# Kernel tuning notes

Hardware: AMD Instinct MI355X
Metric: run time of the kernel (lower is better)

## Reference

```python
import jax, jax.numpy as jnp
import numpy as np

NEG = jnp.float32(-1e30)  # finite stand-in for -inf in masked max
SLOPE = 0.01              # F.leaky_relu default negative slope


def _lrelu(v):
    return jnp.where(v >= 0, v, SLOPE * v)


def _mlp(pts, w1, b1, w2, b2, w3, b3):
    # pts: [2, N] -> [64, N]; 1x1 Conv1d == pointwise linear over channel dim
    z = _lrelu(w1 @ pts + b1[:, None])
    z = _lrelu(w2 @ z + b2[:, None])
    z = _lrelu(w3 @ z + b3[:, None])
    return z


def setup_inputs() -> dict:
    key = jax.random.key(0)
    ks = jax.random.split(key, 10)
    B, C, H, W = 4, 19, 256, 256
    x = jax.random.randint(ks[0], (B, C, H, W), 0, 2, dtype=jnp.int32)
    # grid exactly as in the torch module: meshgrid of two linspaces, flattened
    g = np.array(np.meshgrid(np.linspace(-1, 1, 256), np.linspace(-1, 1, 256),
                             sparse=False)).astype(np.float32)  # [2,256,256]
    grid = jnp.asarray(g.reshape(2, -1))  # [2, 65536]
    w1 = jax.random.normal(ks[1], (64, 2), jnp.float32) * 0.5
    b1 = jax.random.normal(ks[2], (64,), jnp.float32) * 0.1
    w2 = jax.random.normal(ks[3], (64, 64), jnp.float32) * 0.125
    b2 = jax.random.normal(ks[4], (64,), jnp.float32) * 0.1
    w3 = jax.random.normal(ks[5], (64, 64), jnp.float32) * 0.125
    b3 = jax.random.normal(ks[6], (64,), jnp.float32) * 0.1
    fcw = jax.random.normal(ks[7], (512, 64 * C), jnp.float32)
    fcb = jax.random.normal(ks[8], (512,), jnp.float32) * 0.1
    return {"x": x, "grid": grid, "w1": w1, "b1": b1, "w2": w2, "b2": b2,
            "w3": w3, "b3": b3, "fcw": fcw, "fcb": fcb}


def reference(x, grid, w1, b1, w2, b2, w3, b3, fcw, fcb):
    B, C = x.shape[0], x.shape[1]
    # Pointwise MLP on the shared grid once (grid identical for all b,c)
    feats = _mlp(grid, w1, b1, w2, b2, w3, b3)                 # [64, N]
    # Fallback feature for empty masks: MLP on a single zero point
    zero_feat = _mlp(jnp.zeros((2, 1), feats.dtype),
                     w1, b1, w2, b2, w3, b3)[:, 0]             # [64]
    mask = (x.reshape(B, C, -1) == 1)                          # [B, C, N]
    # Masked max over the ragged point sets, fully vectorized
    masked = jnp.where(mask[:, :, None, :], feats[None, None], NEG)
    z = jnp.max(masked, axis=-1)                               # [B, C, 64]
    empty = ~jnp.any(mask, axis=-1)                            # [B, C]
    z = jnp.where(empty[..., None], zero_feat, z)
    flat = z.reshape(B, C * 64)                                # channel-major cat
    # EqualLinear: weight scaled by 1/sqrt(in_dim) (lr_mul=1)
    scale = jnp.float32(1.0 / np.sqrt(C * 64))
    out = flat @ (fcw * scale).T + fcb                         # [B, 512]
    return jnp.repeat(out[:, None, :], 18, axis=1)             # [B, 18, 512]
```

## Files before the change

### kernel.cpp

```cpp
#include <hip/hip_runtime.h>

#define NPTS  65536
#define NBC   76
#define NREP  8
#define KEYN  4864

__device__ __forceinline__ float lrelu(float v) { return fmaxf(v, 0.01f * v); }

__device__ __forceinline__ unsigned fkey(float f) {
  unsigned u = __float_as_uint(f);
  return (u & 0x80000000u) ? ~u : (u | 0x80000000u);
}
__device__ __forceinline__ float fdec(unsigned k) {
  return (k & 0x80000000u) ? __uint_as_float(k & 0x7fffffffu) : __uint_as_float(~k);
}

__global__ __launch_bounds__(512, 8) void k1_fused(
    const int* __restrict__ x, const float* __restrict__ grid,
    const float* __restrict__ w1, const float* __restrict__ b1,
    const float* __restrict__ w2, const float* __restrict__ b2,
    const float* __restrict__ w3, const float* __restrict__ b3,
    unsigned* __restrict__ keys)
{
  __shared__ unsigned zt1[64 * 68];
  __shared__ unsigned zt2[64 * 68];
  __shared__ unsigned long long mbits[NBC];

  const int t    = threadIdx.x;
  const int lane = t & 63;
  const int wv   = t >> 6;
  const int n0   = blockIdx.x * 64;

  #pragma unroll
  for (int i = 0; i < 10; ++i) {
    int bc = wv + 8 * i;
    if (bc < NBC) {
      int v = x[(bc << 16) + n0 + lane];
      unsigned long long m = __ballot(v == 1);
      if (lane == 0) mbits[bc] = m;
    }
  }

  const int jb = __builtin_amdgcn_readfirstlane(wv * 8);

  {
    float g0 = grid[n0 + lane];
    float g1 = grid[NPTS + n0 + lane];
    #pragma unroll
    for (int jj = 0; jj < 8; ++jj) {
      int j = jb + jj;
      float z = lrelu(w1[2 * j] * g0 + w1[2 * j + 1] * g1 + b1[j]);
      zt1[j * 68 + lane] = __float_as_uint(z);
    }
  }
  __syncthreads();

  float acc[8];

  #pragma unroll
  for (int jj = 0; jj < 8; ++jj) acc[jj] = b2[jb + jj];
  #pragma unroll 4
  for (int k = 0; k < 64; ++k) {
    float zv = __uint_as_float(zt1[k * 68 + lane]);
    #pragma unroll
    for (int jj = 0; jj < 8; ++jj) acc[jj] += w2[(jb + jj) * 64 + k] * zv;
  }
  #pragma unroll
  for (int jj = 0; jj < 8; ++jj)
    zt2[(jb + jj) * 68 + lane] = __float_as_uint(lrelu(acc[jj]));
  __syncthreads();

  #pragma unroll
  for (int jj = 0; jj < 8; ++jj) acc[jj] = b3[jb + jj];
  #pragma unroll 4
  for (int k = 0; k < 64; ++k) {
    float zv = __uint_as_float(zt2[k * 68 + lane]);
    #pragma unroll
    for (int jj = 0; jj < 8; ++jj) acc[jj] += w3[(jb + jj) * 64 + k] * zv;
  }
  #pragma unroll
  for (int jj = 0; jj < 8; ++jj)
    zt1[(jb + jj) * 68 + lane] = fkey(lrelu(acc[jj]));
  __syncthreads();

  const int kq = t & 31, bg = t >> 5;
  const int bcbase = bg * 5;

  unsigned mlo[5], mhi[5];
  #pragma unroll
  for (int ii = 0; ii < 5; ++ii) {
    int bc = bcbase + ii;
    unsigned long long m = (bc < NBC) ? mbits[bc] : 0ull;
    mlo[ii] = (unsigned)m;
    mhi[ii] = (unsigned)(m >> 32);
  }

  unsigned uacc[5][2];
  #pragma unroll
  for (int ii = 0; ii < 5; ++ii) { uacc[ii][0] = 0u; uacc[ii][1] = 0u; }

  #pragma unroll 2
  for (int np = 0; np < 8; ++np) {
    const int n = np * 4;
    uint4 lo0 = *reinterpret_cast<const uint4*>(&zt1[kq * 68 + n]);
    uint4 lo1 = *reinterpret_cast<const uint4*>(&zt1[(kq + 32) * 68 + n]);
    uint4 hi0 = *reinterpret_cast<const uint4*>(&zt1[kq * 68 + n + 32]);
    uint4 hi1 = *reinterpret_cast<const uint4*>(&zt1[(kq + 32) * 68 + n + 32]);
    #pragma unroll
    for (int ii = 0; ii < 5; ++ii) {
      unsigned sl0 = (unsigned)((int)(mlo[ii] << (31 - n)) >> 31);
      unsigned sl1 = (unsigned)((int)(mlo[ii] << (30 - n)) >> 31);
      unsigned sl2 = (unsigned)((int)(mlo[ii] << (29 - n)) >> 31);
      unsigned sl3 = (unsigned)((int)(mlo[ii] << (28 - n)) >> 31);
      unsigned sh0 = (unsigned)((int)(mhi[ii] << (31 - n)) >> 31);
      unsigned sh1 = (unsigned)((int)(mhi[ii] << (30 - n)) >> 31);
      unsigned sh2 = (unsigned)((int)(mhi[ii] << (29 - n)) >> 31);
      unsigned sh3 = (unsigned)((int)(mhi[ii] << (28 - n)) >> 31);
      unsigned a0 = uacc[ii][0], a1 = uacc[ii][1];
      a0 = max(max(a0, lo0.x & sl0), lo0.y & sl1);
      a0 = max(max(a0, lo0.z & sl2), lo0.w & sl3);
      a0 = max(max(a0, hi0.x & sh0), hi0.y & sh1);
      a0 = max(max(a0, hi0.z & sh2), hi0.w & sh3);
      a1 = max(max(a1, lo1.x & sl0), lo1.y & sl1);
      a1 = max(max(a1, lo1.z & sl2), lo1.w & sl3);
      a1 = max(max(a1, hi1.x & sh0), hi1.y & sh1);
      a1 = max(max(a1, hi1.z & sh2), hi1.w & sh3);
      uacc[ii][0] = a0; uacc[ii][1] = a1;
    }
  }

  unsigned* krep = keys + (blockIdx.x & (NREP - 1)) * KEYN;
  #pragma unroll
  for (int ii = 0; ii < 5; ++ii) {
    int bc = bcbase + ii;
    if (bc < NBC) {
      unsigned v0 = uacc[ii][0], v1 = uacc[ii][1];
      if (v0) atomicMax(&krep[bc * 64 + kq], v0);
      if (v1) atomicMax(&krep[bc * 64 + kq + 32], v1);
    }
  }
}

__global__ __launch_bounds__(256) void k2_fc(
    const unsigned* __restrict__ keys,
    const float* __restrict__ b1, const float* __restrict__ w2,
    const float* __restrict__ b2, const float* __restrict__ w3,
    const float* __restrict__ b3,
    const float* __restrict__ fcw, const float* __restrict__ fcb,
    float* __restrict__ out)
{
  __shared__ float flat[4864];
  __shared__ float za[64], zb[64], zf[64];
  const int t = threadIdx.x;

  if (t < 64) za[t] = lrelu(b1[t]);
  __syncthreads();
  if (t < 64) {
    float s = b2[t];
    #pragma unroll 8
    for (int k = 0; k < 64; ++k) s += w2[t * 64 + k] * za[k];
    zb[t] = lrelu(s);
  }
  __syncthreads();
  if (t < 64) {
    float s = b3[t];
    #pragma unroll 8
    for (int k = 0; k < 64; ++k) s += w3[t * 64 + k] * zb[k];
    zf[t] = lrelu(s);
  }
  __syncthreads();

  for (int idx = t; idx < 4864; idx += 256) {
    unsigned m = keys[idx];
    #pragma unroll
    for (int r = 1; r < NREP; ++r) m = max(m, keys[r * KEYN + idx]);
    flat[idx] = m ? fdec(m) : zf[idx & 63];
  }
  __syncthreads();

  const int wv = t >> 6, lane = t & 63;
  const int o = blockIdx.x * 4 + wv;
  const float* wrow = fcw + o * 1216;
  float fa0 = 0.f, fa1 = 0.f, fa2 = 0.f, fa3 = 0.f;
  #pragma unroll
  for (int i = 0; i < 19; ++i) {
    int jj = i * 64 + lane;
    float wvv = wrow[jj];
    fa0 += wvv * flat[jj];
    fa1 += wvv * flat[1216 + jj];
    fa2 += wvv * flat[2432 + jj];
    fa3 += wvv * flat[3648 + jj];
  }
  #pragma unroll
  for (int off = 32; off > 0; off >>= 1) {
    fa0 += __shfl_xor(fa0, off);
    fa1 += __shfl_xor(fa1, off);
    fa2 += __shfl_xor(fa2, off);
    fa3 += __shfl_xor(fa3, off);
  }
  const float scale = 0.028676966733820225f;
  float cb = fcb[o];
  if (lane < 18) {
    out[(0 * 18 + lane) * 512 + o] = fa0 * scale + cb;
    out[(1 * 18 + lane) * 512 + o] = fa1 * scale + cb;
    out[(2 * 18 + lane) * 512 + o] = fa2 * scale + cb;
    out[(3 * 18 + lane) * 512 + o] = fa3 * scale + cb;
  }
}

extern "C" void kernel_launch(void* const* d_in, const int* in_sizes, int n_in,
                              void* d_out, int out_size, void* d_ws, size_t ws_size,
                              hipStream_t stream)
{
  const int*   x    = (const int*)d_in[0];
  const float* grid = (const float*)d_in[1];
  const float* w1   = (const float*)d_in[2];
  const float* b1   = (const float*)d_in[3];
  const float* w2   = (const float*)d_in[4];
  const float* b2   = (const float*)d_in[5];
  const float* w3   = (const float*)d_in[6];
  const float* b3   = (const float*)d_in[7];
  const float* fcw  = (const float*)d_in[8];
  const float* fcb  = (const float*)d_in[9];
  float* out = (float*)d_out;

  unsigned* keys = (unsigned*)d_ws;

  hipMemsetAsync(d_ws, 0, NREP * KEYN * sizeof(unsigned), stream);
  hipLaunchKernelGGL(k1_fused, dim3(1024), dim3(512), 0, stream,
                     x, grid, w1, b1, w2, b2, w3, b3, keys);
  hipLaunchKernelGGL(k2_fc, dim3(128), dim3(256), 0, stream,
                     keys, b1, w2, b2, w3, b3, fcw, fcb, out);
}
```

Baseline: 142.2 us.

## Run pointwise MLP layers on fp16 MFMA and pack max keys as 16-bit pairs

```diff
diff --git a/kernel.cpp b/kernel.cpp
--- a/kernel.cpp
+++ b/kernel.cpp
@@ -5,14 +5,28 @@
 #define NREP  8
 #define KEYN  4864
 
+typedef _Float16 f16;
+typedef __fp16   h16x2 __attribute__((ext_vector_type(2)));
+typedef _Float16 f16x8 __attribute__((ext_vector_type(8)));
+typedef float    f32x4 __attribute__((ext_vector_type(4)));
+
 __device__ __forceinline__ float lrelu(float v) { return fmaxf(v, 0.01f * v); }
 
-__device__ __forceinline__ unsigned fkey(float f) {
-  unsigned u = __float_as_uint(f);
-  return (u & 0x80000000u) ? ~u : (u | 0x80000000u);
-}
-__device__ __forceinline__ float fdec(unsigned k) {
-  return (k & 0x80000000u) ? __uint_as_float(k & 0x7fffffffu) : __uint_as_float(~k);
+__device__ __forceinline__ unsigned pkrtz(float lo, float hi) {
+  h16x2 p = __builtin_amdgcn_cvt_pkrtz(lo, hi);
+  return __builtin_bit_cast(unsigned, p);
+}
+__device__ __forceinline__ unsigned pkey(unsigned u) {
+  unsigned t = (u >> 15) & 0x00010001u;
+  return u ^ (0x80008000u | (t * 0x7FFFu));
+}
+__device__ __forceinline__ unsigned pkmax(unsigned a, unsigned b) {
+  unsigned d;
+  asm("v_pk_max_u16 %0, %1, %2" : "=v"(d) : "v"(a), "v"(b));
+  return d;
+}
+__device__ __forceinline__ unsigned sext1(unsigned x, int b) {
+  return (unsigned)(((int)(x << (31 - b))) >> 31);
 }
 
 __global__ __launch_bounds__(512, 8) void k1_fused(
@@ -22,121 +36,144 @@
     const float* __restrict__ w3, const float* __restrict__ b3,
     unsigned* __restrict__ keys)
 {
-  __shared__ unsigned zt1[64 * 68];
-  __shared__ unsigned zt2[64 * 68];
+  __shared__ __align__(16) unsigned char smem[36864];
   __shared__ unsigned long long mbits[NBC];
+  f16* zA  = (f16*)(smem);
+  f16* zB  = (f16*)(smem + 9216);
+  f16* wf2 = (f16*)(smem + 18432);
+  f16* wf3 = (f16*)(smem + 27648);
+  unsigned* zkey = (unsigned*)(smem + 18432);
 
   const int t    = threadIdx.x;
   const int lane = t & 63;
   const int wv   = t >> 6;
   const int n0   = blockIdx.x * 64;
 
+  int xv[10];
   #pragma unroll
   for (int i = 0; i < 10; ++i) {
     int bc = wv + 8 * i;
-    if (bc < NBC) {
-      int v = x[(bc << 16) + n0 + lane];
-      unsigned long long m = __ballot(v == 1);
-      if (lane == 0) mbits[bc] = m;
-    }
-  }
-
-  const int jb = __builtin_amdgcn_readfirstlane(wv * 8);
-
-  {
-    float g0 = grid[n0 + lane];
-    float g1 = grid[NPTS + n0 + lane];
-    #pragma unroll
-    for (int jj = 0; jj < 8; ++jj) {
-      int j = jb + jj;
-      float z = lrelu(w1[2 * j] * g0 + w1[2 * j + 1] * g1 + b1[j]);
-      zt1[j * 68 + lane] = __float_as_uint(z);
-    }
-  }
-  __syncthreads();
-
-  float acc[8];
-
-  #pragma unroll
-  for (int jj = 0; jj < 8; ++jj) acc[jj] = b2[jb + jj];
-  #pragma unroll 4
-  for (int k = 0; k < 64; ++k) {
-    float zv = __uint_as_float(zt1[k * 68 + lane]);
-    #pragma unroll
-    for (int jj = 0; jj < 8; ++jj) acc[jj] += w2[(jb + jj) * 64 + k] * zv;
-  }
-  #pragma unroll
-  for (int jj = 0; jj < 8; ++jj)
-    zt2[(jb + jj) * 68 + lane] = __float_as_uint(lrelu(acc[jj]));
-  __syncthreads();
-
-  #pragma unroll
-  for (int jj = 0; jj < 8; ++jj) acc[jj] = b3[jb + jj];
-  #pragma unroll 4
-  for (int k = 0; k < 64; ++k) {
-    float zv = __uint_as_float(zt2[k * 68 + lane]);
-    #pragma unroll
-    for (int jj = 0; jj < 8; ++jj) acc[jj] += w3[(jb + jj) * 64 + k] * zv;
-  }
-  #pragma unroll
-  for (int jj = 0; jj < 8; ++jj)
-    zt1[(jb + jj) * 68 + lane] = fkey(lrelu(acc[jj]));
-  __syncthreads();
-
-  const int kq = t & 31, bg = t >> 5;
-  const int bcbase = bg * 5;
-
-  unsigned mlo[5], mhi[5];
+    xv[i] = (bc < NBC) ? x[(bc << 16) + n0 + lane] : 0;
+  }
+
+  {
+    int ch = t >> 3, k0 = (t & 7) * 8;
+    const float4* s2 = (const float4*)(w2 + ch * 64 + k0);
+    float4 a = s2[0], b = s2[1];
+    *(uint4*)&wf2[ch * 72 + k0] =
+        make_uint4(pkrtz(a.x, a.y), pkrtz(a.z, a.w), pkrtz(b.x, b.y), pkrtz(b.z, b.w));
+    const float4* s3 = (const float4*)(w3 + ch * 64 + k0);
+    float4 c = s3[0], d = s3[1];
+    *(uint4*)&wf3[ch * 72 + k0] =
+        make_uint4(pkrtz(c.x, c.y), pkrtz(c.z, c.w), pkrtz(d.x, d.y), pkrtz(d.z, d.w));
+  }
+
+  {
+    float g0 = grid[n0 + lane], g1 = grid[NPTS + n0 + lane];
+    unsigned uo[4];
+    #pragma unroll
+    for (int p = 0; p < 4; ++p) {
+      int j = wv * 8 + p * 2;
+      float z0 = lrelu(w1[2 * j] * g0 + w1[2 * j + 1] * g1 + b1[j]);
+      float z1 = lrelu(w1[2 * j + 2] * g0 + w1[2 * j + 3] * g1 + b1[j + 1]);
+      uo[p] = pkrtz(z0, z1);
+    }
+    *(uint4*)&zA[lane * 72 + wv * 8] = make_uint4(uo[0], uo[1], uo[2], uo[3]);
+  }
+  __syncthreads();
+
+  const int chb = (wv & 3) * 16, pth = (wv >> 2) * 32;
+  const int c15 = lane & 15, q = lane >> 4;
+  const int chq = chb + q * 4;
+  const int pt0 = pth + c15, pt1 = pth + 16 + c15;
+
+  f32x4 acc0, acc1;
+
+  {
+    float4 bias = *(const float4*)(b2 + chq);
+    acc0 = (f32x4){bias.x, bias.y, bias.z, bias.w};
+    acc1 = acc0;
+    #pragma unroll
+    for (int k0 = 0; k0 < 64; k0 += 32) {
+      f16x8 af = *(const f16x8*)&wf2[(chb + c15) * 72 + k0 + q * 8];
+      f16x8 b0 = *(const f16x8*)&zA[pt0 * 72 + k0 + q * 8];
+      f16x8 b1f = *(const f16x8*)&zA[pt1 * 72 + k0 + q * 8];
+      acc0 = __builtin_amdgcn_mfma_f32_16x16x32_f16(af, b0, acc0, 0, 0, 0);
+      acc1 = __builtin_amdgcn_mfma_f32_16x16x32_f16(af, b1f, acc1, 0, 0, 0);
+    }
+    *(uint2*)&zB[pt0 * 72 + chq] =
+        make_uint2(pkrtz(lrelu(acc0[0]), lrelu(acc0[1])),
+                   pkrtz(lrelu(acc0[2]), lrelu(acc0[3])));
+    *(uint2*)&zB[pt1 * 72 + chq] =
+        make_uint2(pkrtz(lrelu(acc1[0]), lrelu(acc1[1])),
+                   pkrtz(lrelu(acc1[2]), lrelu(acc1[3])));
+  }
+
+  #pragma unroll
+  for (int i = 0; i < 10; ++i) {
+    int bc = wv + 8 * i;
+    unsigned long long m = __ballot(xv[i] == 1);
+    if (bc < NBC && lane == 0) mbits[bc] = m;
+  }
+  __syncthreads();
+
+  {
+    float4 bias = *(const float4*)(b3 + chq);
+    acc0 = (f32x4){bias.x, bias.y, bias.z, bias.w};
+    acc1 = acc0;
+    #pragma unroll
+    for (int k0 = 0; k0 < 64; k0 += 32) {
+      f16x8 af = *(const f16x8*)&wf3[(chb + c15) * 72 + k0 + q * 8];
+      f16x8 b0 = *(const f16x8*)&zB[pt0 * 72 + k0 + q * 8];
+      f16x8 b1f = *(const f16x8*)&zB[pt1 * 72 + k0 + q * 8];
+      acc0 = __builtin_amdgcn_mfma_f32_16x16x32_f16(af, b0, acc0, 0, 0, 0);
+      acc1 = __builtin_amdgcn_mfma_f32_16x16x32_f16(af, b1f, acc1, 0, 0, 0);
+    }
+    int r0 = chq >> 1;
+    zkey[r0 * 68 + pt0]       = pkey(pkrtz(lrelu(acc0[0]), lrelu(acc0[1])));
+    zkey[(r0 + 1) * 68 + pt0] = pkey(pkrtz(lrelu(acc0[2]), lrelu(acc0[3])));
+    zkey[r0 * 68 + pt1]       = pkey(pkrtz(lrelu(acc1[0]), lrelu(acc1[1])));
+    zkey[(r0 + 1) * 68 + pt1] = pkey(pkrtz(lrelu(acc1[2]), lrelu(acc1[3])));
+  }
+  __syncthreads();
+
+  const int rw = t & 31, bg = t >> 5;
+  const int bc0 = bg * 5;
+
+  unsigned mlo[5], mhi[5], uacc[5];
   #pragma unroll
   for (int ii = 0; ii < 5; ++ii) {
-    int bc = bcbase + ii;
+    int bc = bc0 + ii;
     unsigned long long m = (bc < NBC) ? mbits[bc] : 0ull;
     mlo[ii] = (unsigned)m;
     mhi[ii] = (unsigned)(m >> 32);
-  }
-
-  unsigned uacc[5][2];
-  #pragma unroll
-  for (int ii = 0; ii < 5; ++ii) { uacc[ii][0] = 0u; uacc[ii][1] = 0u; }
-
-  #pragma unroll 2
-  for (int np = 0; np < 8; ++np) {
-    const int n = np * 4;
-    uint4 lo0 = *reinterpret_cast<const uint4*>(&zt1[kq * 68 + n]);
-    uint4 lo1 = *reinterpret_cast<const uint4*>(&zt1[(kq + 32) * 68 + n]);
-    uint4 hi0 = *reinterpret_cast<const uint4*>(&zt1[kq * 68 + n + 32]);
-    uint4 hi1 = *reinterpret_cast<const uint4*>(&zt1[(kq + 32) * 68 + n + 32]);
+    uacc[ii] = 0u;
+  }
+
+  #pragma unroll
+  for (int np = 0; np < 16; ++np) {
+    uint4 z4 = *(const uint4*)&zkey[rw * 68 + np * 4];
+    const int p = np * 4, pb = p & 31;
     #pragma unroll
     for (int ii = 0; ii < 5; ++ii) {
-      unsigned sl0 = (unsigned)((int)(mlo[ii] << (31 - n)) >> 31);
-      unsigned sl1 = (unsigned)((int)(mlo[ii] << (30 - n)) >> 31);
-      unsigned sl2 = (unsigned)((int)(mlo[ii] << (29 - n)) >> 31);
-      unsigned sl3 = (unsigned)((int)(mlo[ii] << (28 - n)) >> 31);
-      unsigned sh0 = (unsigned)((int)(mhi[ii] << (31 - n)) >> 31);
-      unsigned sh1 = (unsigned)((int)(mhi[ii] << (30 - n)) >> 31);
-      unsigned sh2 = (unsigned)((int)(mhi[ii] << (29 - n)) >> 31);
-      unsigned sh3 = (unsigned)((int)(mhi[ii] << (28 - n)) >> 31);
-      unsigned a0 = uacc[ii][0], a1 = uacc[ii][1];
-      a0 = max(max(a0, lo0.x & sl0), lo0.y & sl1);
-      a0 = max(max(a0, lo0.z & sl2), lo0.w & sl3);
-      a0 = max(max(a0, hi0.x & sh0), hi0.y & sh1);
-      a0 = max(max(a0, hi0.z & sh2), hi0.w & sh3);
-      a1 = max(max(a1, lo1.x & sl0), lo1.y & sl1);
-      a1 = max(max(a1, lo1.z & sl2), lo1.w & sl3);
-      a1 = max(max(a1, hi1.x & sh0), hi1.y & sh1);
-      a1 = max(max(a1, hi1.z & sh2), hi1.w & sh3);
-      uacc[ii][0] = a0; uacc[ii][1] = a1;
+      unsigned m = (p < 32) ? mlo[ii] : mhi[ii];
+      unsigned s0 = sext1(m, pb),     s1 = sext1(m, pb + 1);
+      unsigned s2 = sext1(m, pb + 2), s3 = sext1(m, pb + 3);
+      unsigned a = uacc[ii];
+      a = pkmax(a, z4.x & s0); a = pkmax(a, z4.y & s1);
+      a = pkmax(a, z4.z & s2); a = pkmax(a, z4.w & s3);
+      uacc[ii] = a;
     }
   }
 
   unsigned* krep = keys + (blockIdx.x & (NREP - 1)) * KEYN;
   #pragma unroll
   for (int ii = 0; ii < 5; ++ii) {
-    int bc = bcbase + ii;
+    int bc = bc0 + ii;
     if (bc < NBC) {
-      unsigned v0 = uacc[ii][0], v1 = uacc[ii][1];
-      if (v0) atomicMax(&krep[bc * 64 + kq], v0);
-      if (v1) atomicMax(&krep[bc * 64 + kq + 32], v1);
+      unsigned lo = uacc[ii] & 0xFFFFu, hi = uacc[ii] >> 16;
+      if (lo) atomicMax(&krep[bc * 64 + 2 * rw], lo);
+      if (hi) atomicMax(&krep[bc * 64 + 2 * rw + 1], hi);
     }
   }
 }
@@ -174,7 +211,15 @@
     unsigned m = keys[idx];
     #pragma unroll
     for (int r = 1; r < NREP; ++r) m = max(m, keys[r * KEYN + idx]);
-    flat[idx] = m ? fdec(m) : zf[idx & 63];
+    float v;
+    if (m) {
+      unsigned u = (m & 0x8000u) ? (m ^ 0x8000u) : (~m & 0xFFFFu);
+      unsigned short us = (unsigned short)u;
+      v = (float)__builtin_bit_cast(f16, us);
+    } else {
+      v = zf[idx & 63];
+    }
+    flat[idx] = v;
   }
   __syncthreads();
 
@@ -226,7 +271,7 @@
 
   unsigned* keys = (unsigned*)d_ws;
 
-  hipMemsetAsync(d_ws, 0, NREP * KEYN * sizeof(unsigned), stream);
+  (void)hipMemsetAsync(d_ws, 0, NREP * KEYN * sizeof(unsigned), stream);
   hipLaunchKernelGGL(k1_fused, dim3(1024), dim3(512), 0, stream,
                      x, grid, w1, b1, w2, b2, w3, b3, keys);
   hipLaunchKernelGGL(k2_fc, dim3(128), dim3(256), 0, stream,
```

Result: faster. 129.8 us (-8.7%).
